# Kernel tuning notes

Hardware: AMD Instinct MI355X
Metric: run time of the kernel (lower is better)

Reference implementation:

```python
import jax, jax.numpy as jnp
import numpy as np

IN_C, OUT_C = 32, 64
KSIZE = (3, 3, 3)


def setup_inputs() -> dict:
    key = jax.random.key(0)
    k1, k2 = jax.random.split(key)
    x = jax.random.normal(k1, (2, IN_C, 64, 64, 64), dtype=jnp.float32)
    # One learnable scalar per (out_channel, in_channel, kz, ky, kx) basis function.
    W = jax.random.normal(k2, (OUT_C, IN_C) + KSIZE, dtype=jnp.float32) * 0.05
    return {"x": x, "W": W}


def reference(x, W):
    # Original: for each (oc, ic, kz, ky, kx), out[:, oc] += basis(x[:, ic, shifted_slices])
    # With scalar-weight bases this is exactly a VALID (unpadded) 3D convolution:
    # out[b, o, d, h, w] = sum_{i, kz, ky, kx} W[o, i, kz, ky, kx] * x[b, i, d+kz, h+ky, w+kx]
    return jax.lax.conv_general_dilated(
        x, W,
        window_strides=(1, 1, 1),
        padding="VALID",
        dimension_numbers=("NCDHW", "OIDHW", "NCDHW"),
    )
```

## Files before the change

kernel.cpp:

```cpp
#include <hip/hip_runtime.h>
#include <hip/hip_bf16.h>

#define DIN 64
#define DOUT 62
#define ICH 32
#define OCH 64

typedef __bf16 bf16x8 __attribute__((ext_vector_type(8)));
typedef float f32x4 __attribute__((ext_vector_type(4)));
typedef float f32x8 __attribute__((ext_vector_type(8)));
typedef float f32x16 __attribute__((ext_vector_type(16)));

#define AS1U(p) ((const __attribute__((address_space(1))) unsigned int*)(p))
#define AS3U(p) ((__attribute__((address_space(3))) unsigned int*)(p))

__global__ void prep_all(const float* __restrict__ x, const float* __restrict__ W,
                         unsigned short* __restrict__ Wre3, unsigned short* __restrict__ xp) {
    const int bid = blockIdx.x;
    if (bid < 8192) {
        int idx = bid * 256 + threadIdx.x;
        int w = idx & 63;
        int s = (idx >> 6) & 3;
        int y = (idx >> 8) & 63;
        int z = (idx >> 14) & 63;
        int b = idx >> 20;
        const float* xb = x + ((size_t)(b * ICH + s * 8)) * 262144 + (size_t)z * 4096 + y * 64 + w;
        bf16x8 pk;
#pragma unroll
        for (int j = 0; j < 8; ++j)
            pk[j] = (__bf16)xb[(size_t)j * 262144];
        ((int4*)xp)[idx] = __builtin_bit_cast(int4, pk);
    } else {
        int idx = (bid - 8192) * 256 + threadIdx.x;
        if (idx < 27 * OCH * ICH) {
            int j    = idx & 7;
            int lane = (idx >> 3) & 63;
            int kh   = (idx >> 9) & 1;
            int mt   = (idx >> 10) & 1;
            int tap  = idx >> 11;
            int oc   = mt * 32 + (lane & 31);
            int ic   = kh * 16 + (lane >> 5) * 8 + j;
            float v  = W[((size_t)oc * ICH + ic) * 27 + tap];
            Wre3[idx] = __builtin_bit_cast(unsigned short, (__bf16)v);
        }
    }
}

__global__ __launch_bounds__(512, 4) void conv3d_mfma_pk(
    const unsigned short* __restrict__ Wre3,
    const unsigned short* __restrict__ xp,
    float* __restrict__ out)
{
    __shared__ char xs[2 * 24576 + 256];

    const int tid  = threadIdx.x;
    const int lane = tid & 63;
    const int wave = tid >> 6;
    const int rloc  = wave & 3;
    const int ohalf = wave >> 2;

    const int orig = blockIdx.x;
    const int lid  = (orig & 7) * 248 + (orig >> 3);
    const int ht = lid & 15;
    const int rr = lid >> 4;
    const int d  = rr % DOUT;
    const int b  = rr / DOUT;
    const int h0 = ht * 4;

    const int l31 = lane & 31;
    const int lhi = lane >> 5;

    auto stage_chunk = [&](char* buf, int z, int i) {
        int c  = wave * 3 + i;
        int yl = c >> 2;
        int sl = c & 3;
        int srow = h0 + yl; if (srow > 63) srow = 63;
        const unsigned short* src =
            xp + ((((size_t)(b * DIN + z) * DIN + srow) * 4 + sl) * 64) * 8 + lane * 8;
        __builtin_amdgcn_global_load_lds(AS1U(src), AS3U(buf + c * 1024), 16, 0, 0);
    };
    auto loadA = [&](int tap, int4* af) {
        const int4* wp = (const int4*)Wre3 + (size_t)tap * 256 + ohalf * 128 + lane;
#pragma unroll
        for (int kh = 0; kh < 2; ++kh)
            af[kh] = wp[kh * 64];
    };
    auto readB = [&](const char* buf, int ky, int kx, int4* dst) {
#pragma unroll
        for (int kh = 0; kh < 2; ++kh) {
            const int g = kh * 2 + lhi;
#pragma unroll
            for (int nt = 0; nt < 2; ++nt) {
                int wb = nt * 32 + l31 + kx;
                if (wb > 63) wb = 63;
                dst[kh * 2 + nt] = *(const int4*)(buf + (((rloc + ky) * 4 + g) * 64 + wb) * 16);
            }
        }
    };

    char* bufA = xs;
    char* bufB = xs + 24576;

#pragma unroll
    for (int i = 0; i < 3; ++i) stage_chunk(bufA, d, i);
    int4 af[3][2];
    loadA(0, af[0]);
    loadA(1, af[1]);

    f32x16 acc[2];
#pragma unroll
    for (int nt = 0; nt < 2; ++nt)
#pragma unroll
        for (int r = 0; r < 16; ++r) acc[nt][r] = 0.f;

    __syncthreads();

    int4 bfr[2][4];
    const bool oddw = (wave & 1) != 0;

#pragma unroll
    for (int kz = 0; kz < 3; ++kz) {
        char* cur = (kz & 1) ? bufB : bufA;
        char* nxt = (kz & 1) ? bufA : bufB;
        readB(cur, 0, 0, bfr[0]);

#pragma unroll
        for (int t = 0; t < 9; ++t) {
            const int T = kz * 9 + t;
            if (oddw) {
                if (t < 8)  readB(cur, (t + 1) / 3, (t + 1) % 3, bfr[(t + 1) & 1]);
                if (T < 25) loadA(T + 2, af[(T + 2) % 3]);
            } else {
                if (T < 25) loadA(T + 2, af[(T + 2) % 3]);
                if (t < 8)  readB(cur, (t + 1) / 3, (t + 1) % 3, bfr[(t + 1) & 1]);
            }
            if (kz < 2 && t < 3) stage_chunk(nxt, d + kz + 1, t);

#pragma unroll
            for (int kh = 0; kh < 2; ++kh)
#pragma unroll
                for (int nt = 0; nt < 2; ++nt)
                    acc[nt] = __builtin_amdgcn_mfma_f32_32x32x16_bf16(
                        __builtin_bit_cast(bf16x8, af[T % 3][kh]),
                        __builtin_bit_cast(bf16x8, bfr[t & 1][kh * 2 + nt]),
                        acc[nt], 0, 0, 0);
        }
        if (kz < 2) __syncthreads();
    }

    const int h = h0 + rloc;
    if (h < DOUT) {
#pragma unroll
        for (int r = 0; r < 16; ++r) {
            int oc = ohalf * 32 + (r & 3) + 8 * (r >> 2) + 4 * lhi;
            size_t ob = ((((size_t)b * OCH + oc) * DOUT + d) * DOUT + h) * DOUT;
#pragma unroll
            for (int nt = 0; nt < 2; ++nt) {
                int ww = nt * 32 + l31;
                if (ww < DOUT) out[ob + ww] = acc[nt][r];
            }
        }
    }
}

__global__ __launch_bounds__(256, 3) void conv3d_mfma_fb(
    const float* __restrict__ x, const float* __restrict__ W,
    float* __restrict__ out)
{
    __shared__ char xs[2][6 * 66 * 64];

    const int tid  = threadIdx.x;
    const int lane = tid & 63;
    const int wave = tid >> 6;

    const int orig = blockIdx.x;
    const int lid  = (orig & 7) * 248 + (orig >> 3);
    const int ht = lid & 15;
    const int rr = lid >> 4;
    const int d  = rr % DOUT;
    const int b  = rr / DOUT;
    const int h0 = ht * 4;

    const int wlo = lane & 15;
    const int whi = lane >> 4;
    const int row = wave;

    const int icg  = wave;
    const int w    = lane;
    const int slot = icg ^ ((w >> 1) & 3);

    auto issueRow = [&](int z, int y) -> f32x8 {
        int gy = h0 + y; if (gy > 63) gy = 63;
        const float* xp2 = x + (((size_t)(b * ICH + icg * 8) * DIN + z) * DIN + gy) * DIN + w;
        f32x8 s;
#pragma unroll
        for (int j = 0; j < 8; ++j) s[j] = xp2[(size_t)j * DIN * DIN * DIN];
        return s;
    };
    auto writeRow = [&](char* buf, int y, f32x8 s) {
        bf16x8 pk;
#pragma unroll
        for (int j = 0; j < 8; ++j) pk[j] = (__bf16)s[j];
        *(int4*)(buf + ((y * 66 + w) * 64 + slot * 16)) = __builtin_bit_cast(int4, pk);
    };
    auto loadA = [&](int tap, int4* af) {
#pragma unroll
        for (int mt = 0; mt < 4; ++mt) {
            const float* wp = W + ((size_t)(mt * 16 + wlo) * ICH + whi * 8) * 27 + tap;
            bf16x8 t;
#pragma unroll
            for (int j = 0; j < 8; ++j) t[j] = (__bf16)wp[j * 27];
            af[mt] = __builtin_bit_cast(int4, t);
        }
    };
    auto readB = [&](const char* buf, int ky, int kx, int4* dst) {
#pragma unroll
        for (int nt = 0; nt < 4; ++nt) {
            int wb = nt * 16 + wlo + kx;
            int sl = whi ^ ((wb >> 1) & 3);
            dst[nt] = *(const int4*)(buf + (((row + ky) * 66 + wb) * 64 + sl * 16));
        }
    };

    if (tid < 96) {
        int bu = tid / 48, q2 = tid % 48;
        int y = q2 >> 3, q = q2 & 7;
        int w2 = 64 + (q >> 2), sl = q & 3;
        *(int4*)(xs[bu] + ((y * 66 + w2) * 64 + sl * 16)) = int4{0, 0, 0, 0};
    }
    {
        f32x8 s0 = issueRow(d, 0), s1 = issueRow(d, 1), s2 = issueRow(d, 2);
        writeRow(xs[0], 0, s0); s0 = issueRow(d, 3);
        writeRow(xs[0], 1, s1); s1 = issueRow(d, 4);
        writeRow(xs[0], 2, s2); s2 = issueRow(d, 5);
        writeRow(xs[0], 3, s0); writeRow(xs[0], 4, s1); writeRow(xs[0], 5, s2);
    }
    int4 af[2][4];
    loadA(0, af[0]);
    __syncthreads();

    f32x4 acc[4][4];
#pragma unroll
    for (int mt = 0; mt < 4; ++mt)
#pragma unroll
        for (int nt = 0; nt < 4; ++nt)
            acc[mt][nt] = f32x4{0.f, 0.f, 0.f, 0.f};

    int4 bfr[2][4];

#pragma unroll
    for (int kz = 0; kz < 3; ++kz) {
        char* cur = xs[kz & 1];
        char* nxt = xs[(kz + 1) & 1];
        f32x8 s0, s1, s2;
        readB(cur, 0, 0, bfr[0]);
#pragma unroll
        for (int t = 0; t < 9; ++t) {
            const int T = kz * 9 + t;
            if (T < 26) loadA(T + 1, af[(T + 1) & 1]);
            if (t < 8)  readB(cur, (t + 1) / 3, (t + 1) % 3, bfr[(t + 1) & 1]);
            if (kz < 2) {
                if (t == 3) writeRow(nxt, 0, s0);
                if (t == 4) writeRow(nxt, 1, s1);
                if (t == 5) writeRow(nxt, 2, s2);
                if (t == 6) writeRow(nxt, 3, s0);
                if (t == 7) writeRow(nxt, 4, s1);
                if (t == 8) writeRow(nxt, 5, s2);
                if (t == 0) s0 = issueRow(d + kz + 1, 0);
                if (t == 1) s1 = issueRow(d + kz + 1, 1);
                if (t == 2) s2 = issueRow(d + kz + 1, 2);
                if (t == 3) s0 = issueRow(d + kz + 1, 3);
                if (t == 4) s1 = issueRow(d + kz + 1, 4);
                if (t == 5) s2 = issueRow(d + kz + 1, 5);
            }
#pragma unroll
            for (int mt = 0; mt < 4; ++mt)
#pragma unroll
                for (int nt = 0; nt < 4; ++nt)
                    acc[mt][nt] = __builtin_amdgcn_mfma_f32_16x16x32_bf16(
                        __builtin_bit_cast(bf16x8, af[T & 1][mt]),
                        __builtin_bit_cast(bf16x8, bfr[t & 1][nt]),
                        acc[mt][nt], 0, 0, 0);
        }
        if (kz < 2) __syncthreads();
    }

    const int h = h0 + row;
    if (h < DOUT) {
#pragma unroll
        for (int mt = 0; mt < 4; ++mt) {
#pragma unroll
            for (int r = 0; r < 4; ++r) {
                int oc = mt * 16 + whi * 4 + r;
                size_t ob = ((((size_t)b * OCH + oc) * DOUT + d) * DOUT + h) * DOUT;
#pragma unroll
                for (int nt = 0; nt < 4; ++nt) {
                    int ww = nt * 16 + wlo;
                    if (ww < DOUT) out[ob + ww] = acc[mt][nt][r];
                }
            }
        }
    }
}

extern "C" void kernel_launch(void* const* d_in, const int* in_sizes, int n_in,
                              void* d_out, int out_size, void* d_ws, size_t ws_size,
                              hipStream_t stream) {
    const float* x = (const float*)d_in[0];
    const float* W = (const float*)d_in[1];
    float* out = (float*)d_out;

    const size_t wre_elems = (size_t)27 * OCH * ICH;
    const size_t xp_elems  = (size_t)2 * DIN * DIN * DIN * ICH;
    const size_t need = (wre_elems + xp_elems) * 2 + 256;

    if (ws_size >= need) {
        unsigned short* Wre3 = (unsigned short*)d_ws;
        unsigned short* xp   = Wre3 + wre_elems;
        prep_all<<<dim3(8192 + 216), 256, 0, stream>>>(x, W, Wre3, xp);
        conv3d_mfma_pk<<<dim3(2 * DOUT * 16), 512, 0, stream>>>(Wre3, xp, out);
    } else {
        conv3d_mfma_fb<<<dim3(2 * DOUT * 16), 256, 0, stream>>>(x, W, out);
    }
}
```

Measured before the change: 88.80 us.

## Compute two output depth slices per block to reuse staged input planes

```diff
diff --git a/kernel.cpp b/kernel.cpp
--- a/kernel.cpp
+++ b/kernel.cpp
@@ -46,118 +46,132 @@
     }
 }
 
-__global__ __launch_bounds__(512, 4) void conv3d_mfma_pk(
+__global__ __launch_bounds__(256, 3) void conv3d_mfma_pk(
     const unsigned short* __restrict__ Wre3,
     const unsigned short* __restrict__ xp,
     float* __restrict__ out)
 {
-    __shared__ char xs[2 * 24576 + 256];
+    __shared__ char xs[2 * 16384 + 256];
 
     const int tid  = threadIdx.x;
     const int lane = tid & 63;
     const int wave = tid >> 6;
-    const int rloc  = wave & 3;
-    const int ohalf = wave >> 2;
+    const int rloc  = wave & 1;
+    const int ohalf = wave >> 1;
 
     const int orig = blockIdx.x;
-    const int lid  = (orig & 7) * 248 + (orig >> 3);
-    const int ht = lid & 15;
-    const int rr = lid >> 4;
-    const int d  = rr % DOUT;
-    const int b  = rr / DOUT;
-    const int h0 = ht * 4;
+    const int xcd  = orig & 7;
+    const int kk   = orig >> 3;
+    const int lid  = (xcd < 2 ? xcd * 241 : 482 + (xcd - 2) * 240) + kk;
+    const int ht = lid % 31;
+    const int rr = lid / 31;
+    const int dp = rr % 31;
+    const int b  = rr / 31;
+    const int d0 = dp * 2;
+    const int h0 = ht * 2;
 
     const int l31 = lane & 31;
     const int lhi = lane >> 5;
 
     auto stage_chunk = [&](char* buf, int z, int i) {
-        int c  = wave * 3 + i;
+        int c  = wave * 4 + i;
         int yl = c >> 2;
         int sl = c & 3;
-        int srow = h0 + yl; if (srow > 63) srow = 63;
         const unsigned short* src =
-            xp + ((((size_t)(b * DIN + z) * DIN + srow) * 4 + sl) * 64) * 8 + lane * 8;
+            xp + ((((size_t)(b * DIN + z) * DIN + (h0 + yl)) * 4 + sl) * 64) * 8 + lane * 8;
         __builtin_amdgcn_global_load_lds(AS1U(src), AS3U(buf + c * 1024), 16, 0, 0);
     };
-    auto loadA = [&](int tap, int4* af) {
+    auto loadA = [&](int tap, int4* a2) {
         const int4* wp = (const int4*)Wre3 + (size_t)tap * 256 + ohalf * 128 + lane;
-#pragma unroll
-        for (int kh = 0; kh < 2; ++kh)
-            af[kh] = wp[kh * 64];
+        a2[0] = wp[0];
+        a2[1] = wp[64];
     };
     auto readB = [&](const char* buf, int ky, int kx, int4* dst) {
 #pragma unroll
         for (int kh = 0; kh < 2; ++kh) {
-            const int g = kh * 2 + lhi;
+            const int sg = kh * 2 + lhi;
 #pragma unroll
             for (int nt = 0; nt < 2; ++nt) {
                 int wb = nt * 32 + l31 + kx;
                 if (wb > 63) wb = 63;
-                dst[kh * 2 + nt] = *(const int4*)(buf + (((rloc + ky) * 4 + g) * 64 + wb) * 16);
-            }
-        }
-    };
-
-    char* bufA = xs;
-    char* bufB = xs + 24576;
-
-#pragma unroll
-    for (int i = 0; i < 3; ++i) stage_chunk(bufA, d, i);
-    int4 af[3][2];
-    loadA(0, af[0]);
-    loadA(1, af[1]);
-
-    f32x16 acc[2];
-#pragma unroll
-    for (int nt = 0; nt < 2; ++nt)
-#pragma unroll
-        for (int r = 0; r < 16; ++r) acc[nt][r] = 0.f;
+                dst[kh * 2 + nt] = *(const int4*)(buf + (((rloc + ky) * 4 + sg) * 64 + wb) * 16);
+            }
+        }
+    };
+
+#pragma unroll
+    for (int i = 0; i < 4; ++i) stage_chunk(xs, d0, i);
+    int4 afA[2][2], afB[2][2];
+    loadA(0, afA[0]);
+
+    f32x16 acc[2][2];
+#pragma unroll
+    for (int o = 0; o < 2; ++o)
+#pragma unroll
+        for (int nt = 0; nt < 2; ++nt)
+#pragma unroll
+            for (int r = 0; r < 16; ++r) acc[o][nt][r] = 0.f;
 
     __syncthreads();
 
     int4 bfr[2][4];
-    const bool oddw = (wave & 1) != 0;
-
-#pragma unroll
-    for (int kz = 0; kz < 3; ++kz) {
-        char* cur = (kz & 1) ? bufB : bufA;
-        char* nxt = (kz & 1) ? bufA : bufB;
+
+#pragma unroll
+    for (int s = 0; s < 4; ++s) {
+        char* cur = xs + (s & 1) * 16384;
+        char* nxt = xs + ((s + 1) & 1) * 16384;
         readB(cur, 0, 0, bfr[0]);
 
 #pragma unroll
-        for (int t = 0; t < 9; ++t) {
-            const int T = kz * 9 + t;
-            if (oddw) {
-                if (t < 8)  readB(cur, (t + 1) / 3, (t + 1) % 3, bfr[(t + 1) & 1]);
-                if (T < 25) loadA(T + 2, af[(T + 2) % 3]);
-            } else {
-                if (T < 25) loadA(T + 2, af[(T + 2) % 3]);
-                if (t < 8)  readB(cur, (t + 1) / 3, (t + 1) % 3, bfr[(t + 1) & 1]);
-            }
-            if (kz < 2 && t < 3) stage_chunk(nxt, d + kz + 1, t);
-
-#pragma unroll
-            for (int kh = 0; kh < 2; ++kh)
-#pragma unroll
-                for (int nt = 0; nt < 2; ++nt)
-                    acc[nt] = __builtin_amdgcn_mfma_f32_32x32x16_bf16(
-                        __builtin_bit_cast(bf16x8, af[T % 3][kh]),
-                        __builtin_bit_cast(bf16x8, bfr[t & 1][kh * 2 + nt]),
-                        acc[nt], 0, 0, 0);
-        }
-        if (kz < 2) __syncthreads();
+        for (int it = 0; it < 9; ++it) {
+            const int g = s * 9 + it;
+            const int p = g & 1;
+
+            if (g < 35) {
+                const int sn  = (it == 8) ? s + 1 : s;
+                const int itn = (it == 8) ? 0 : it + 1;
+                if (sn <= 2) loadA(sn * 9 + itn, afA[p ^ 1]);
+                if (sn >= 1) loadA((sn - 1) * 9 + itn, afB[p ^ 1]);
+            }
+            if (it < 8) readB(cur, (it + 1) / 3, (it + 1) % 3, bfr[(it + 1) & 1]);
+            if (s < 3 && it < 4) stage_chunk(nxt, d0 + s + 1, it);
+
+            if (s <= 2) {
+#pragma unroll
+                for (int kh = 0; kh < 2; ++kh)
+#pragma unroll
+                    for (int nt = 0; nt < 2; ++nt)
+                        acc[0][nt] = __builtin_amdgcn_mfma_f32_32x32x16_bf16(
+                            __builtin_bit_cast(bf16x8, afA[p][kh]),
+                            __builtin_bit_cast(bf16x8, bfr[it & 1][kh * 2 + nt]),
+                            acc[0][nt], 0, 0, 0);
+            }
+            if (s >= 1) {
+#pragma unroll
+                for (int kh = 0; kh < 2; ++kh)
+#pragma unroll
+                    for (int nt = 0; nt < 2; ++nt)
+                        acc[1][nt] = __builtin_amdgcn_mfma_f32_32x32x16_bf16(
+                            __builtin_bit_cast(bf16x8, afB[p][kh]),
+                            __builtin_bit_cast(bf16x8, bfr[it & 1][kh * 2 + nt]),
+                            acc[1][nt], 0, 0, 0);
+            }
+        }
+        if (s < 3) __syncthreads();
     }
 
     const int h = h0 + rloc;
-    if (h < DOUT) {
+#pragma unroll
+    for (int o = 0; o < 2; ++o) {
+        const int dd = d0 + o;
 #pragma unroll
         for (int r = 0; r < 16; ++r) {
             int oc = ohalf * 32 + (r & 3) + 8 * (r >> 2) + 4 * lhi;
-            size_t ob = ((((size_t)b * OCH + oc) * DOUT + d) * DOUT + h) * DOUT;
+            size_t ob = ((((size_t)b * OCH + oc) * DOUT + dd) * DOUT + h) * DOUT;
 #pragma unroll
             for (int nt = 0; nt < 2; ++nt) {
                 int ww = nt * 32 + l31;
-                if (ww < DOUT) out[ob + ww] = acc[nt][r];
+                if (ww < DOUT) out[ob + ww] = acc[o][nt][r];
             }
         }
     }
@@ -318,7 +332,7 @@
         unsigned short* Wre3 = (unsigned short*)d_ws;
         unsigned short* xp   = Wre3 + wre_elems;
         prep_all<<<dim3(8192 + 216), 256, 0, stream>>>(x, W, Wre3, xp);
-        conv3d_mfma_pk<<<dim3(2 * DOUT * 16), 512, 0, stream>>>(Wre3, xp, out);
+        conv3d_mfma_pk<<<dim3(2 * 31 * 31), 256, 0, stream>>>(Wre3, xp, out);
     } else {
         conv3d_mfma_fb<<<dim3(2 * DOUT * 16), 256, 0, stream>>>(x, W, out);
     }
```

Result: faster. 85.29 us (-4.0%).
